# Optimization experiments

Measured on AMD Instinct MI355X. Metric: run time of the kernel, lower is better.

The kernel has to match this reference:

```python
import jax, jax.numpy as jnp
import numpy as np

N = 8192
D_IN = 512
D_OUT = 256
K = 16          # k_neighbor
ALPHA = 0.5
BETA = 1.0


def get_M(H, beta, k):
    """Cholesky-whitened kNN Gaussian-kernel graph, symmetrized. H: [N, d]."""
    d = H.shape[1]
    A = beta * jnp.eye(d, dtype=H.dtype) + H.T @ H            # [d, d]
    L = jnp.linalg.cholesky(A)                                # lower, A = L L^T
    # norm_covariance = H @ inv(L).T  ==  (L^{-1} H^T)^T
    Z = jax.scipy.linalg.solve_triangular(L, H.T, lower=True).T  # [N, d]
    sq = jnp.sum(Z * Z, axis=1)
    d2 = sq[:, None] + sq[None, :] - 2.0 * (Z @ Z.T)          # [N, N] squared dists
    neg_d2, idx = jax.lax.top_k(-d2, k)                       # k smallest
    vals = jnp.sqrt(jnp.clip(-neg_d2, 0.0))                   # [N, k]
    sigma = jnp.mean(vals)
    kern = jnp.exp(-(vals * vals) / (2.0 * sigma * sigma))
    n = Z.shape[0]
    rows = jnp.repeat(jnp.arange(n), k)
    M = jnp.zeros((n, n), Z.dtype).at[rows, idx.reshape(-1)].add(kern.reshape(-1))
    return 0.5 * (M + M.T)


def normalize_adj(M):
    deg = jnp.sum(M, axis=1)
    dis = jnp.where(deg > 0, deg ** -0.5, 0.0)
    return dis[:, None] * M * dis[None, :]


def setup_inputs() -> dict:
    key = jax.random.key(0)
    k1, k2, k3, k4 = jax.random.split(key, 4)
    lim1 = float(np.sqrt(6.0 / (D_IN + D_OUT)))
    lim2 = float(np.sqrt(6.0 / (D_OUT + D_OUT)))
    return {
        "x": jax.random.normal(k1, (N, D_IN), dtype=jnp.float32),
        "adj": jax.random.uniform(k2, (N, N), dtype=jnp.float32),
        "weight1": jax.random.uniform(k3, (D_IN, D_OUT), dtype=jnp.float32, minval=-lim1, maxval=lim1),
        "weight2": jax.random.uniform(k4, (D_OUT, D_OUT), dtype=jnp.float32, minval=-lim2, maxval=lim2),
    }


def reference(x, adj, weight1, weight2):
    # stage 1: build whitened kNN graph from detached x
    M1 = get_M(jax.lax.stop_gradient(x), BETA, K)
    new_adj = ALPHA * adj + normalize_adj(M1)
    out = jnp.tanh(new_adj @ (x @ weight1))                   # [N, D_OUT]
    # stage 2: rebuild graph from detached hidden, symmetrize weight2
    M2 = get_M(jax.lax.stop_gradient(out), BETA, K)
    new_adj2 = ALPHA * adj + normalize_adj(M2)
    w2_sym = 0.5 * (weight2 + weight2.T)
    out = jnp.tanh(new_adj2 @ (out @ w2_sym))
    return out
```

## Files before the change

### kernel.cpp

```cpp
#include <hip/hip_runtime.h>
#include <math.h>
#include <float.h>

#define N_TOT 8192
#define KNB 16
#define ALPHA 0.5f
#define PROWS 2048
#define NCH 8
#define KS 4

typedef short bf16x8 __attribute__((ext_vector_type(8)));
typedef float f32x4 __attribute__((ext_vector_type(4)));

__device__ inline unsigned short f2bf(float f) {
    unsigned u = __float_as_uint(f);
    u += 0x7fffu + ((u >> 16) & 1u);
    return (unsigned short)(u >> 16);
}
__device__ inline float bf2f(unsigned short h) {
    return __uint_as_float(((unsigned)h) << 16);
}

__global__ __launch_bounds__(256)
void k_ata2(const float* __restrict__ H, double* __restrict__ Apart, int d) {
    __shared__ float Ha[32][33], Hb[32][33];
    int tid = threadIdx.x, tx = tid&15, ty = tid>>4;
    int a0 = blockIdx.y*32, b0 = blockIdx.x*32;
    int n0b = blockIdx.z*(N_TOT/NCH);
    int lrow = tid>>3, lseg = tid&7;
    double acc[2][2];
    acc[0][0]=acc[0][1]=acc[1][0]=acc[1][1]=0.0;
    for (int n0 = n0b; n0 < n0b + N_TOT/NCH; n0 += 32) {
        float4 va = *(const float4*)&H[(long)(n0+lrow)*d + a0 + lseg*4];
        float4 vb = *(const float4*)&H[(long)(n0+lrow)*d + b0 + lseg*4];
        __syncthreads();
        Ha[lrow][lseg*4+0]=va.x; Ha[lrow][lseg*4+1]=va.y;
        Ha[lrow][lseg*4+2]=va.z; Ha[lrow][lseg*4+3]=va.w;
        Hb[lrow][lseg*4+0]=vb.x; Hb[lrow][lseg*4+1]=vb.y;
        Hb[lrow][lseg*4+2]=vb.z; Hb[lrow][lseg*4+3]=vb.w;
        __syncthreads();
        float f00=0.f,f01=0.f,f10=0.f,f11=0.f;
        #pragma unroll
        for (int nn = 0; nn < 32; ++nn) {
            float a0v = Ha[nn][ty*2], a1v = Ha[nn][ty*2+1];
            float b0v = Hb[nn][tx*2], b1v = Hb[nn][tx*2+1];
            f00 = fmaf(a0v,b0v,f00); f01 = fmaf(a0v,b1v,f01);
            f10 = fmaf(a1v,b0v,f10); f11 = fmaf(a1v,b1v,f11);
        }
        acc[0][0]+= (double)f00; acc[0][1]+= (double)f01;
        acc[1][0]+= (double)f10; acc[1][1]+= (double)f11;
    }
    long base = (long)blockIdx.z*d*d;
    #pragma unroll
    for (int i=0;i<2;++i)
        #pragma unroll
        for (int j=0;j<2;++j)
            Apart[base + (long)(a0+ty*2+i)*d + b0+tx*2+j] = acc[i][j];
}

__global__ __launch_bounds__(256)
void k_atared(const double* __restrict__ Apart, double* __restrict__ A,
              int d, double beta) {
    long idx = (long)blockIdx.x*256 + threadIdx.x;
    long dd = (long)d*d;
    double s = 0.0;
    for (int ch = 0; ch < NCH; ++ch) s += Apart[ch*dd + idx];
    int r = (int)(idx / d), c = (int)(idx % d);
    A[idx] = s + ((r==c) ? beta : 0.0);
}

__global__ __launch_bounds__(64)
void k_chol_diag(double* __restrict__ A, int d, int p0) {
    __shared__ double Ad[64][65];
    int r = threadIdx.x;
    for (int idx = r; idx < 64*64; idx += 64)
        Ad[idx>>6][idx&63] = A[(long)(p0+(idx>>6))*d + p0+(idx&63)];
    __syncthreads();
    for (int j = 0; j < 64; ++j) {
        double pj = sqrt(Ad[j][j]);
        double lrj = Ad[r][j] / pj;
        __syncthreads();
        if (r > j) Ad[r][j] = lrj;
        else if (r == j) Ad[j][j] = pj;
        __syncthreads();
        if (r > j)
            for (int k = j+1; k <= r; ++k)
                Ad[r][k] -= lrj * Ad[k][j];
        __syncthreads();
    }
    for (int idx = r; idx < 64*64; idx += 64) {
        int i = idx>>6, c = idx&63;
        A[(long)(p0+i)*d + p0+c] = (c <= i) ? Ad[i][c] : 0.0;
    }
}

__global__ __launch_bounds__(256)
void k_trsm(double* __restrict__ A, int d, int p0) {
    __shared__ double Lp[64][65];
    __shared__ double dg[64];
    int tid = threadIdx.x;
    for (int idx = tid; idx < 64*64; idx += 256) {
        int j = idx>>6, k = idx&63;
        double v = A[(long)(p0+j)*d + p0+k];
        Lp[j][k] = (j > k) ? v : 0.0;
        if (j == k) dg[j] = v;
    }
    __syncthreads();
    int r = p0 + 64 + blockIdx.x*256 + tid;
    if (r >= d) return;
    double* Ar = &A[(long)r*d + p0];
    double v[64];
    #pragma unroll
    for (int j = 0; j < 64; ++j) v[j] = Ar[j];
    #pragma unroll
    for (int k = 0; k < 64; ++k) {
        double lr = v[k] / dg[k];
        Ar[k] = lr;
        #pragma unroll
        for (int j = 0; j < 64; ++j) v[j] -= lr * Lp[j][k];
    }
}

__global__ __launch_bounds__(256)
void k_syrk(double* __restrict__ A, int d, int p0) {
    int t0 = p0 + 64;
    int r0 = t0 + blockIdx.y*64, c0 = t0 + blockIdx.x*64;
    __shared__ double Lr[64][33], Lc[64][33];
    int tid = threadIdx.x, tx = tid&15, ty = tid>>4;
    double acc[16];
    #pragma unroll
    for (int i=0;i<16;++i) acc[i]=0.0;
    for (int kc = 0; kc < 64; kc += 32) {
        for (int idx = tid; idx < 64*32; idx += 256) {
            int i = idx>>5, k = idx&31;
            Lr[i][k] = A[(long)(r0+i)*d + p0+kc+k];
            Lc[i][k] = A[(long)(c0+i)*d + p0+kc+k];
        }
        __syncthreads();
        for (int k = 0; k < 32; ++k) {
            double a[4], b[4];
            #pragma unroll
            for (int i=0;i<4;++i){ a[i]=Lr[ty*4+i][k]; b[i]=Lc[tx*4+i][k]; }
            #pragma unroll
            for (int i=0;i<4;++i)
                #pragma unroll
                for (int j=0;j<4;++j) acc[i*4+j] += a[i]*b[j];
        }
        __syncthreads();
    }
    #pragma unroll
    for (int i=0;i<4;++i)
        #pragma unroll
        for (int j=0;j<4;++j)
            A[(long)(r0+ty*4+i)*d + (c0+tx*4+j)] -= acc[i*4+j];
}

__global__ __launch_bounds__(64)
void k_dinv(const double* __restrict__ A, double* __restrict__ X, int d) {
    __shared__ double Lb[64][65];
    __shared__ double Yb[64][65];
    int b = blockIdx.x, c = threadIdx.x;
    for (int r = 0; r < 64; ++r) Lb[r][c] = A[(long)(b*64+r)*d + b*64+c];
    for (int r = 0; r < 64; ++r) Yb[r][c] = 0.0;
    __syncthreads();
    for (int i = 0; i < 64; ++i) {
        double s = (i==c) ? 1.0 : 0.0;
        for (int k = 0; k < i; ++k) s -= Lb[i][k]*Yb[k][c];
        Yb[i][c] = s / Lb[i][i];
    }
    __syncthreads();
    for (int r = 0; r < 64; ++r) X[(long)(b*64+r)*d + b*64+c] = Yb[r][c];
}

__global__ __launch_bounds__(256)
void k_xoff(const double* __restrict__ A, double* __restrict__ X, int d, int lev) {
    __shared__ double Lb[64][65];
    __shared__ double Xb[64][65];
    __shared__ double Sb[64][65];
    int j = blockIdx.x, i = j + lev;
    int tid = threadIdx.x, tx = tid&15, ty = tid>>4;
    double acc[4][4];
    #pragma unroll
    for (int m=0;m<4;++m)
        #pragma unroll
        for (int n=0;n<4;++n) acc[m][n]=0.0;
    for (int k = j; k < i; ++k) {
        __syncthreads();
        for (int idx = tid; idx < 64*64; idx += 256) {
            int r = idx>>6, cc = idx&63;
            Lb[r][cc] = A[(long)(i*64+r)*d + k*64+cc];
            Xb[r][cc] = X[(long)(k*64+r)*d + j*64+cc];
        }
        __syncthreads();
        for (int kk = 0; kk < 64; ++kk) {
            double a_[4], b_[4];
            #pragma unroll
            for (int m=0;m<4;++m) a_[m] = Lb[ty*4+m][kk];
            #pragma unroll
            for (int n=0;n<4;++n) b_[n] = Xb[kk][tx*4+n];
            #pragma unroll
            for (int m=0;m<4;++m)
                #pragma unroll
                for (int n=0;n<4;++n) acc[m][n] += a_[m]*b_[n];
        }
    }
    __syncthreads();
    #pragma unroll
    for (int m=0;m<4;++m)
        #pragma unroll
        for (int n=0;n<4;++n) Sb[ty*4+m][tx*4+n] = acc[m][n];
    for (int idx = tid; idx < 64*64; idx += 256) {
        int r = idx>>6, cc = idx&63;
        Lb[r][cc] = X[(long)(i*64+r)*d + i*64+cc];
    }
    __syncthreads();
    #pragma unroll
    for (int m=0;m<4;++m)
        #pragma unroll
        for (int n=0;n<4;++n) acc[m][n]=0.0;
    for (int kk = 0; kk < 64; ++kk) {
        double a_[4], b_[4];
        #pragma unroll
        for (int m=0;m<4;++m) a_[m] = Lb[ty*4+m][kk];
        #pragma unroll
        for (int n=0;n<4;++n) b_[n] = Sb[kk][tx*4+n];
        #pragma unroll
        for (int m=0;m<4;++m)
            #pragma unroll
            for (int n=0;n<4;++n) acc[m][n] += a_[m]*b_[n];
    }
    #pragma unroll
    for (int m=0;m<4;++m)
        #pragma unroll
        for (int n=0;n<4;++n)
            X[(long)(i*64+ty*4+m)*d + j*64+tx*4+n] = -acc[m][n];
}

__global__ __launch_bounds__(256)
void k_wtr(const double* __restrict__ X, double* __restrict__ W, int d, int shift) {
    int idx = blockIdx.x*256 + threadIdx.x;
    int k = idx >> shift, c = idx & (d-1);
    W[idx] = (k <= c) ? X[(long)c*d + k] : 0.0;
}

__global__ __launch_bounds__(256)
void k_hw(const float* __restrict__ H, const double* __restrict__ W,
          float* __restrict__ Z, int d) {
    __shared__ __align__(16) float Ht[32][68];
    __shared__ double Wt[32][66];
    int tid = threadIdx.x, tx = tid&15, ty = tid>>4;
    int r0 = blockIdx.y*64, c0 = blockIdx.x*64;
    double acc[4][4];
    #pragma unroll
    for (int i=0;i<4;++i)
        #pragma unroll
        for (int j=0;j<4;++j) acc[i][j]=0.0;
    for (int k0 = 0; k0 < d; k0 += 32) {
        {
            int row = tid>>2, koff = (tid&3)*8;
            const float* src = &H[(long)(r0+row)*d + k0+koff];
            float4 v0 = *(const float4*)src, v1 = *(const float4*)(src+4);
            Ht[koff+0][row]=v0.x; Ht[koff+1][row]=v0.y; Ht[koff+2][row]=v0.z; Ht[koff+3][row]=v0.w;
            Ht[koff+4][row]=v1.x; Ht[koff+5][row]=v1.y; Ht[koff+6][row]=v1.z; Ht[koff+7][row]=v1.w;
        }
        {
            int k = tid>>3, coff = (tid&7)*8;
            const double* src = &W[(long)(k0+k)*d + c0+coff];
            #pragma unroll
            for (int q=0;q<8;++q) Wt[k][coff+q] = src[q];
        }
        __syncthreads();
        #pragma unroll
        for (int k = 0; k < 32; ++k) {
            float4 av = *(const float4*)&Ht[k][ty*4];
            double a0=av.x, a1=av.y, a2=av.z, a3=av.w;
            double b[4];
            #pragma unroll
            for (int j=0;j<4;++j) b[j] = Wt[k][tx*4+j];
            #pragma unroll
            for (int j=0;j<4;++j) {
                acc[0][j] += a0*b[j]; acc[1][j] += a1*b[j];
                acc[2][j] += a2*b[j]; acc[3][j] += a3*b[j];
            }
        }
        __syncthreads();
    }
    #pragma unroll
    for (int i=0;i<4;++i)
        #pragma unroll
        for (int j=0;j<4;++j)
            Z[(long)(r0+ty*4+i)*d + c0+tx*4+j] = (float)acc[i][j];
}

__global__ __launch_bounds__(256)
void k_sq(const float* __restrict__ Z, float* __restrict__ sq, int d) {
    int row = blockIdx.x*4 + (threadIdx.x>>6);
    int lane = threadIdx.x&63;
    const float* z = &Z[(long)row*d];
    double s = 0.0;
    for (int c = lane; c < d; c += 64) { float v = z[c]; s += (double)v*v; }
    #pragma unroll
    for (int off=32; off>0; off>>=1) s += __shfl_down(s, off);
    if (lane==0) sq[row] = (float)s;
}

__global__ __launch_bounds__(256)
void k_bf16(const float* __restrict__ Z, unsigned short* __restrict__ Zh, long n) {
    long i = ((long)blockIdx.x*256 + threadIdx.x)*8;
    if (i >= n) return;
    float4 v0 = *(const float4*)&Z[i], v1 = *(const float4*)&Z[i+4];
    float z[8] = {v0.x,v0.y,v0.z,v0.w,v1.x,v1.y,v1.z,v1.w};
    __align__(16) unsigned short h[8];
    #pragma unroll
    for (int j=0;j<8;++j) h[j] = f2bf(z[j]);
    *(uint4*)&Zh[i] = *(const uint4*)h;
}

__global__ __launch_bounds__(256)
void k_gram(const unsigned short* __restrict__ Zh, const float* __restrict__ sq,
            float* __restrict__ d2, int d, int prow0) {
    __shared__ unsigned short At[128*64], Bt[128*64];
    int tid = threadIdx.x, w = tid>>6, lane = tid&63;
    int lr = lane&15, kg = lane>>4;
    int wr = w>>1, wc = w&1;
    int r0 = prow0 + blockIdx.y*128;
    int c0 = blockIdx.x*128;
    f32x4 acc[4][4];
    #pragma unroll
    for (int m=0;m<4;++m)
        #pragma unroll
        for (int n=0;n<4;++n) acc[m][n] = (f32x4){0.f,0.f,0.f,0.f};

    for (int k0 = 0; k0 < d; k0 += 64) {
        __syncthreads();
        #pragma unroll
        for (int ii=0; ii<4; ++ii) {
            int rbase = w*32 + ii*8;
            int grow = rbase + (lane>>3);
            int gg = (lane&7) ^ (grow&7);
            __builtin_amdgcn_global_load_lds((const void*)&Zh[(long)(r0+grow)*d + k0 + gg*8],
                                             (void*)&At[rbase*64], 16, 0, 0);
            __builtin_amdgcn_global_load_lds((const void*)&Zh[(long)(c0+grow)*d + k0 + gg*8],
                                             (void*)&Bt[rbase*64], 16, 0, 0);
        }
        __syncthreads();
        #pragma unroll
        for (int ks=0; ks<2; ++ks) {
            int gsw = ((ks<<2)|kg) ^ (lr&7);
            bf16x8 a_[4];
            #pragma unroll
            for (int m=0;m<4;++m) a_[m] = *(const bf16x8*)&At[(wr*64+m*16+lr)*64 + gsw*8];
            #pragma unroll
            for (int n=0;n<4;++n) {
                bf16x8 b_ = *(const bf16x8*)&Bt[(wc*64+n*16+lr)*64 + gsw*8];
                #pragma unroll
                for (int m=0;m<4;++m)
                    acc[m][n] = __builtin_amdgcn_mfma_f32_16x16x32_bf16(a_[m], b_, acc[m][n], 0,0,0);
            }
        }
    }
    float sr[4][4];
    #pragma unroll
    for (int m=0;m<4;++m)
        #pragma unroll
        for (int q=0;q<4;++q) sr[m][q] = sq[r0 + wr*64 + m*16 + kg*4 + q];
    #pragma unroll
    for (int n=0;n<4;++n) {
        int col = c0 + wc*64 + n*16 + lr;
        float sc = sq[col];
        #pragma unroll
        for (int m=0;m<4;++m) {
            int rloc = (r0 - prow0) + wr*64 + m*16 + kg*4;
            #pragma unroll
            for (int q=0;q<4;++q)
                d2[(long)(rloc+q)*N_TOT + col] = sr[m][q] + sc - 2.f*acc[m][n][q];
        }
    }
}

__global__ __launch_bounds__(256)
void k_sel(const float* __restrict__ d2, int* __restrict__ tI32, int prow0) {
    __shared__ float cbv[320];
    __shared__ int   cbi[320];
    __shared__ int   red[4];
    __shared__ int   cnt_s;
    __shared__ float fD[32];
    __shared__ int   fI[32];
    int tid = threadIdx.x, w = tid>>6, lane = tid&63;
    int row = blockIdx.x;
    const float* rp = &d2[(long)row*N_TOT];
    float v[32];
    #pragma unroll
    for (int j=0;j<8;++j) {
        float4 q = *(const float4*)&rp[j*1024 + tid*4];
        v[j*4+0]=q.x; v[j*4+1]=q.y; v[j*4+2]=q.z; v[j*4+3]=q.w;
    }
    unsigned u[32];
    #pragma unroll
    for (int i=0;i<32;++i) {
        unsigned b = __float_as_uint(v[i]);
        u[i] = (b & 0x80000000u) ? ~b : (b | 0x80000000u);
    }
    unsigned p = 0;
    for (int b = 31; b >= 0; --b) {
        unsigned t = p | (1u<<b);
        int c = 0;
        #pragma unroll
        for (int i=0;i<32;++i) c += (u[i] < t) ? 1 : 0;
        #pragma unroll
        for (int off=1; off<64; off<<=1) c += __shfl_xor(c, off);
        if (lane == 0) red[w] = c;
        __syncthreads();
        c = red[0]+red[1]+red[2]+red[3];
        if (c < 32) p = t;
        __syncthreads();
    }
    if (tid == 0) cnt_s = 0;
    __syncthreads();
    #pragma unroll
    for (int i=0;i<32;++i) {
        if (u[i] <= p) {
            int pos = atomicAdd(&cnt_s, 1);
            if (pos < 320) { cbv[pos] = v[i]; cbi[pos] = (i>>2)*1024 + tid*4 + (i&3); }
        }
    }
    __syncthreads();
    if (tid == 0) {
        int m = cnt_s; if (m > 320) m = 320;
        #pragma unroll
        for (int k=0;k<32;++k){ fD[k]=FLT_MAX; fI[k]=k; }
        for (int t = 0; t < m; ++t) {
            float dv = cbv[t]; int ci = cbi[t];
            float wd = fD[31]; int wi = fI[31];
            if (dv < wd || (dv == wd && ci < wi)) {
                int pos = 31;
                while (pos > 0) {
                    float pd_=fD[pos-1]; int pi_=fI[pos-1];
                    if (dv < pd_ || (dv == pd_ && ci < pi_)) { fD[pos]=pd_; fI[pos]=pi_; --pos; }
                    else break;
                }
                fD[pos]=dv; fI[pos]=ci;
            }
        }
        long rg = (long)(prow0 + row);
        #pragma unroll
        for (int k=0;k<32;++k) tI32[rg*32 + k] = fI[k];
    }
}

template<int D>
__global__ __launch_bounds__(256)
void k_refine(const float* __restrict__ Z, const float* __restrict__ sq,
              const int* __restrict__ tI32,
              float* __restrict__ tD, int* __restrict__ tI, double* sig_accum) {
    __shared__ float rD[4][32];
    __shared__ int   rI[4][32];
    __shared__ float bD[4][17];
    __shared__ int   bI[4][17];
    int wv = threadIdx.x>>6, lane = threadIdx.x&63;
    long row = (long)blockIdx.x*4 + wv;
    float zi[D/64];
    #pragma unroll
    for (int t=0;t<D/64;++t) zi[t] = Z[row*D + t*64 + lane];
    float sqi = sq[row];
    for (int c = 0; c < 32; ++c) {
        int j = tI32[row*32 + c];
        float dot = 0.f;
        #pragma unroll
        for (int t=0;t<D/64;++t) dot = fmaf(zi[t], Z[(long)j*D + t*64 + lane], dot);
        #pragma unroll
        for (int off=32; off>0; off>>=1) dot += __shfl_xor(dot, off);
        if (lane == 0) { rD[wv][c] = sqi + sq[j] - 2.f*dot; rI[wv][c] = j; }
    }
    if (lane == 0) {
        #pragma unroll
        for (int k=0;k<16;++k){ bD[wv][k]=FLT_MAX; bI[wv][k]=0x7fffffff; }
        for (int c = 0; c < 32; ++c) {
            float dv = rD[wv][c]; int ci = rI[wv][c];
            float wd = bD[wv][15]; int wi = bI[wv][15];
            if (dv < wd || (dv == wd && ci < wi)) {
                int pos = 15;
                while (pos > 0) {
                    float pd_ = bD[wv][pos-1]; int pi_ = bI[wv][pos-1];
                    if (dv < pd_ || (dv == pd_ && ci < pi_)) {
                        bD[wv][pos]=pd_; bI[wv][pos]=pi_; --pos;
                    } else break;
                }
                bD[wv][pos]=dv; bI[wv][pos]=ci;
            }
        }
        double ps = 0.0;
        #pragma unroll
        for (int k=0;k<16;++k) {
            float dv = bD[wv][k];
            tD[row*16+k] = dv; tI[row*16+k] = bI[wv][k];
            ps += sqrt((double)fmaxf(dv, 0.f));
        }
        atomicAdd(sig_accum, ps);
    }
}

__global__ void k_sigfin(const double* __restrict__ sig_accum, float* __restrict__ inv2s2) {
    double s = sig_accum[0] / (double)(N_TOT*KNB);
    inv2s2[0] = (float)(1.0/(2.0*s*s));
}

__global__ __launch_bounds__(256)
void k_kern(const float* __restrict__ tD, const int* __restrict__ tI,
            const float* __restrict__ inv2s2,
            float* __restrict__ kern, float* __restrict__ deg) {
    int e = blockIdx.x*256 + threadIdx.x;
    int i = e>>4;
    float d2 = fmaxf(tD[e], 0.f);
    float kv = expf(-d2 * inv2s2[0]);
    kern[e] = kv;
    atomicAdd(&deg[i], 0.5f*kv);
    atomicAdd(&deg[tI[e]], 0.5f*kv);
}

__global__ __launch_bounds__(256)
void k_dis(const float* __restrict__ deg, float* __restrict__ dis) {
    int i = blockIdx.x*256 + threadIdx.x;
    float v = deg[i];
    dis[i] = (v > 0.f) ? (1.0f/sqrtf(v)) : 0.f;
}

__global__ __launch_bounds__(256)
void k_wedge(const float* __restrict__ kern, const int* __restrict__ tI,
             const float* __restrict__ dis, float* __restrict__ wout) {
    int e = blockIdx.x*256 + threadIdx.x;
    wout[e] = 0.5f * kern[e] * dis[tI[e]];
}

__global__ __launch_bounds__(256)
void k_count(const int* __restrict__ tI, int* __restrict__ cnt) {
    int e = blockIdx.x*256 + threadIdx.x;
    atomicAdd(&cnt[tI[e]], 1);
}

__global__ __launch_bounds__(1024)
void k_scan(const int* __restrict__ cnt, int* __restrict__ rowstart) {
    __shared__ int buf[1024];
    __shared__ int carry;
    int tid = threadIdx.x;
    if (tid==0) carry = 0;
    __syncthreads();
    for (int base = 0; base < N_TOT; base += 1024) {
        int v = cnt[base+tid];
        buf[tid]=v; __syncthreads();
        for (int off=1; off<1024; off<<=1) {
            int t = (tid>=off)? buf[tid-off] : 0; __syncthreads();
            buf[tid]+=t; __syncthreads();
        }
        rowstart[base+tid] = carry + buf[tid] - v;
        __syncthreads();
        if (tid==1023) carry += buf[1023];
        __syncthreads();
    }
    if (tid==0) rowstart[N_TOT] = carry;
}

__global__ __launch_bounds__(256)
void k_fill(const int* __restrict__ tI, const float* __restrict__ kern,
            const float* __restrict__ dis,
            const int* __restrict__ rowstart, int* __restrict__ c2,
            int* __restrict__ in_src, float* __restrict__ in_w) {
    int e = blockIdx.x*256 + threadIdx.x;
    int i = e>>4;
    int j = tI[e];
    int pos = atomicAdd(&c2[j], 1);
    int dst = rowstart[j] + pos;
    in_src[dst] = i; in_w[dst] = 0.5f*kern[e]*dis[i];
}

__global__ __launch_bounds__(256)
void k_gemm(const float* __restrict__ A, const float* __restrict__ B,
            float* __restrict__ C, int M, int N, int Kd, float scale) {
    __shared__ __align__(16) float At[16][68];
    __shared__ __align__(16) float Bt[16][68];
    int tid = threadIdx.x, tx = tid&15, ty = tid>>4;
    int r0 = blockIdx.y*64, c0 = blockIdx.x*64;
    float acc[4][4];
    #pragma unroll
    for (int i=0;i<4;++i)
        #pragma unroll
        for (int j=0;j<4;++j) acc[i][j]=0.f;
    for (int k0 = 0; k0 < Kd; k0 += 16) {
        {
            int row = tid>>2, koff = (tid&3)*4;
            float4 v = *(const float4*)&A[(long)(r0+row)*Kd + k0+koff];
            At[koff+0][row]=v.x; At[koff+1][row]=v.y; At[koff+2][row]=v.z; At[koff+3][row]=v.w;
        }
        {
            int k = tid>>4, coff = (tid&15)*4;
            float4 v = *(const float4*)&B[(long)(k0+k)*N + c0+coff];
            *(float4*)&Bt[k][coff] = v;
        }
        __syncthreads();
        #pragma unroll
        for (int k=0;k<16;++k) {
            float4 a = *(const float4*)&At[k][ty*4];
            float4 b = *(const float4*)&Bt[k][tx*4];
            float ar[4] = {a.x,a.y,a.z,a.w};
            float br[4] = {b.x,b.y,b.z,b.w};
            #pragma unroll
            for (int i=0;i<4;++i)
                #pragma unroll
                for (int j=0;j<4;++j) acc[i][j] = fmaf(ar[i], br[j], acc[i][j]);
        }
        __syncthreads();
    }
    #pragma unroll
    for (int i=0;i<4;++i)
        #pragma unroll
        for (int j=0;j<4;++j)
            C[(long)(r0+ty*4+i)*N + c0+tx*4+j] = scale*acc[i][j];
}

__global__ __launch_bounds__(256)
void k_prepPT(const float* __restrict__ P, unsigned short* __restrict__ PTsh,
              unsigned short* __restrict__ PTsl) {
    __shared__ float tile[64][65];
    int r0 = blockIdx.y*64;
    int c0 = blockIdx.x*64;
    int t = threadIdx.x;
    {
        int row = t>>2, cseg = t&3;
        #pragma unroll
        for (int i=0;i<4;++i) {
            float4 v = *(const float4*)&P[(long)(r0+row)*256 + c0 + cseg*16 + i*4];
            tile[row][cseg*16+i*4+0]=v.x; tile[row][cseg*16+i*4+1]=v.y;
            tile[row][cseg*16+i*4+2]=v.z; tile[row][cseg*16+i*4+3]=v.w;
        }
    }
    __syncthreads();
    {
        int col = t>>2, rseg = t&3;
        int c = c0 + col;
        __align__(16) unsigned short hs[16], ls[16];
        #pragma unroll
        for (int i=0;i<16;++i) {
            float z = tile[rseg*16+i][col];
            hs[i] = f2bf(z);
            ls[i] = f2bf(z - bf2f(hs[i]));
        }
        #pragma unroll
        for (int half=0; half<2; ++half) {
            int gl = rseg*2 + half;
            int gs = gl ^ (c&7);
            long dst = (long)c*N_TOT + r0 + gs*8;
            *(uint4*)&PTsh[dst] = *(const uint4*)&hs[half*8];
            *(uint4*)&PTsl[dst] = *(const uint4*)&ls[half*8];
        }
    }
}

__global__ __launch_bounds__(256)
void k_adjP3(const float* __restrict__ adj, const unsigned short* __restrict__ PTsh,
             const unsigned short* __restrict__ PTsl, float* __restrict__ part) {
    __shared__ unsigned short Ah[64*64], Al[64*64];
    __shared__ unsigned short Bh[128*64], Bl[128*64];
    int tid = threadIdx.x, w = tid>>6, lane = tid&63;
    int lr = lane&15, kg = lane>>4;
    int r0 = blockIdx.y*64;
    int c0 = blockIdx.x*128;
    int kbeg = blockIdx.z*(N_TOT/KS), kend = kbeg + N_TOT/KS;
    f32x4 acc[8];
    #pragma unroll
    for (int fc=0; fc<8; ++fc) acc[fc] = (f32x4){0.f,0.f,0.f,0.f};

    int arow = tid>>2, aseg = tid&3;
    float4 va[4];
    {
        const float* asrc = &adj[(long)(r0+arow)*N_TOT + kbeg + aseg*16];
        #pragma unroll
        for (int i=0;i<4;++i) va[i] = *(const float4*)&asrc[i*4];
    }
    for (int k0 = kbeg; k0 < kend; k0 += 64) {
        __syncthreads();
        #pragma unroll
        for (int i=0;i<4;++i) {
            float z[4] = {va[i].x, va[i].y, va[i].z, va[i].w};
            __align__(8) unsigned short h[4], l[4];
            #pragma unroll
            for (int j=0;j<4;++j) {
                h[j] = f2bf(z[j]);
                l[j] = f2bf(z[j] - bf2f(h[j]));
            }
            int col = aseg*16 + i*4;
            int g = col>>3, sub = col&7;
            int off = arow*128 + ((g ^ (arow&7))*16) + sub*2;
            *(ushort4*)((char*)Ah + off) = *(const ushort4*)h;
            *(ushort4*)((char*)Al + off) = *(const ushort4*)l;
        }
        #pragma unroll
        for (int ii=0; ii<4; ++ii) {
            int rbase = w*32 + ii*8;
            int grow = rbase + (lane>>3);
            long src = (long)(c0+grow)*N_TOT + k0 + (lane&7)*8;
            __builtin_amdgcn_global_load_lds((const void*)&PTsh[src], (void*)&Bh[rbase*64], 16, 0, 0);
            __builtin_amdgcn_global_load_lds((const void*)&PTsl[src], (void*)&Bl[rbase*64], 16, 0, 0);
        }
        __syncthreads();
        if (k0 + 64 < kend) {
            const float* asrc = &adj[(long)(r0+arow)*N_TOT + k0 + 64 + aseg*16];
            #pragma unroll
            for (int i=0;i<4;++i) va[i] = *(const float4*)&asrc[i*4];
        }
        #pragma unroll
        for (int ks=0; ks<2; ++ks) {
            int gsw = ((ks<<2)|kg) ^ (lr&7);
            bf16x8 ah = *(const bf16x8*)&Ah[(w*16+lr)*64 + gsw*8];
            bf16x8 al = *(const bf16x8*)&Al[(w*16+lr)*64 + gsw*8];
            #pragma unroll
            for (int fc=0; fc<8; ++fc) {
                bf16x8 bh = *(const bf16x8*)&Bh[(fc*16+lr)*64 + gsw*8];
                bf16x8 bl = *(const bf16x8*)&Bl[(fc*16+lr)*64 + gsw*8];
                acc[fc] = __builtin_amdgcn_mfma_f32_16x16x32_bf16(ah, bh, acc[fc], 0,0,0);
                acc[fc] = __builtin_amdgcn_mfma_f32_16x16x32_bf16(ah, bl, acc[fc], 0,0,0);
                acc[fc] = __builtin_amdgcn_mfma_f32_16x16x32_bf16(al, bh, acc[fc], 0,0,0);
            }
        }
    }
    long base = (long)blockIdx.z*N_TOT*256;
    #pragma unroll
    for (int fc=0; fc<8; ++fc)
        #pragma unroll
        for (int q=0; q<4; ++q) {
            int rg = r0 + w*16 + kg*4 + q;
            int cg = c0 + fc*16 + lr;
            part[base + (long)rg*256 + cg] = acc[fc][q];
        }
}

__global__ __launch_bounds__(256)
void k_adjred(const float* __restrict__ part, float* __restrict__ preS, float scale) {
    long i4 = ((long)blockIdx.x*256 + threadIdx.x)*4;
    long n = (long)N_TOT*256;
    float4 a = *(const float4*)&part[i4];
    float4 b = *(const float4*)&part[n + i4];
    float4 c = *(const float4*)&part[2*n + i4];
    float4 d = *(const float4*)&part[3*n + i4];
    float4 o;
    o.x = scale*(((a.x + b.x) + c.x) + d.x);
    o.y = scale*(((a.y + b.y) + c.y) + d.y);
    o.z = scale*(((a.z + b.z) + c.z) + d.z);
    o.w = scale*(((a.w + b.w) + c.w) + d.w);
    *(float4*)&preS[i4] = o;
}

__global__ __launch_bounds__(256)
void k_wsym(const float* __restrict__ w2, float* __restrict__ w2s) {
    int i = blockIdx.x, j = threadIdx.x;
    w2s[i*256+j] = 0.5f*(w2[i*256+j] + w2[j*256+i]);
}

__global__ __launch_bounds__(256)
void k_spmm_tanh(const float* __restrict__ P, const float* __restrict__ preS,
                 const float* __restrict__ wout, const int* __restrict__ tI,
                 const float* __restrict__ dis, const int* __restrict__ rowstart,
                 const int* __restrict__ in_src, const float* __restrict__ in_w,
                 float* __restrict__ out) {
    int i = blockIdx.x, c = threadIdx.x;
    float a0=0.f, a1=0.f, a2=0.f, a3=0.f;
    #pragma unroll
    for (int k = 0; k < 16; k += 4) {
        int e = i*16+k;
        int j0 = tI[e+0], j1 = tI[e+1], j2 = tI[e+2], j3 = tI[e+3];
        float w0 = wout[e+0], w1 = wout[e+1], w2 = wout[e+2], w3 = wout[e+3];
        a0 = fmaf(w0, P[(long)j0*256 + c], a0);
        a1 = fmaf(w1, P[(long)j1*256 + c], a1);
        a2 = fmaf(w2, P[(long)j2*256 + c], a2);
        a3 = fmaf(w3, P[(long)j3*256 + c], a3);
    }
    int s0 = rowstart[i], s1 = rowstart[i+1];
    int t = s0;
    for (; t + 4 <= s1; t += 4) {
        int j0 = in_src[t+0], j1 = in_src[t+1], j2 = in_src[t+2], j3 = in_src[t+3];
        float w0 = in_w[t+0], w1 = in_w[t+1], w2 = in_w[t+2], w3 = in_w[t+3];
        a0 = fmaf(w0, P[(long)j0*256 + c], a0);
        a1 = fmaf(w1, P[(long)j1*256 + c], a1);
        a2 = fmaf(w2, P[(long)j2*256 + c], a2);
        a3 = fmaf(w3, P[(long)j3*256 + c], a3);
    }
    for (; t < s1; ++t)
        a0 = fmaf(in_w[t], P[(long)in_src[t]*256 + c], a0);
    float acc = (a0 + a1) + (a2 + a3);
    float pre = preS[(long)i*256+c] + dis[i]*acc;
    out[(long)i*256+c] = tanhf(pre);
}

extern "C" void kernel_launch(void* const* d_in, const int* in_sizes, int n_in,
                              void* d_out, int out_size, void* d_ws, size_t ws_size,
                              hipStream_t stream) {
    const float* x   = (const float*)d_in[0];
    const float* adj = (const float*)d_in[1];
    const float* w1  = (const float*)d_in[2];
    const float* w2  = (const float*)d_in[3];

    char* ws = (char*)d_ws;
    size_t off = 0;
    auto alloc = [&](size_t bytes){ size_t o = off; off += (bytes+255)&~(size_t)255; return o; };
    double* A      = (double*)(ws + alloc((size_t)512*512*8));
    double* W      = (double*)(ws + alloc((size_t)512*512*8));
    double* Xb     = (double*)(ws + alloc((size_t)512*512*8));
    double* Apart  = (double*)(ws + alloc((size_t)NCH*512*512*8));
    double* sigacc = (double*)(ws + alloc(256));
    float*  inv2s2 = (float*)(ws + alloc(256));
    float*  bigZ   = (float*)(ws + alloc((size_t)N_TOT*512*4));
    unsigned short* Zh   = (unsigned short*)(ws + alloc((size_t)N_TOT*512*2));
    unsigned short* PTsh = (unsigned short*)(ws + alloc((size_t)256*N_TOT*2));
    unsigned short* PTsl = (unsigned short*)(ws + alloc((size_t)256*N_TOT*2));
    float*  d2buf  = (float*)(ws + alloc((size_t)PROWS*N_TOT*4));
    float*  part   = (float*)(ws + alloc((size_t)KS*N_TOT*256*4));
    float*  sq     = (float*)(ws + alloc((size_t)N_TOT*4));
    int*    tI32   = (int*)  (ws + alloc((size_t)N_TOT*32*4));
    float*  tD     = (float*)(ws + alloc((size_t)N_TOT*16*4));
    int*    tI     = (int*)  (ws + alloc((size_t)N_TOT*16*4));
    float*  kern   = (float*)(ws + alloc((size_t)N_TOT*16*4));
    float*  wout   = (float*)(ws + alloc((size_t)N_TOT*16*4));
    float*  deg    = (float*)(ws + alloc((size_t)N_TOT*4));
    float*  dis    = (float*)(ws + alloc((size_t)N_TOT*4));
    int*    cnt    = (int*)  (ws + alloc((size_t)N_TOT*4));
    int*    rowstart=(int*)  (ws + alloc((size_t)(N_TOT+1)*4));
    int*    c2     = (int*)  (ws + alloc((size_t)N_TOT*4));
    int*    in_src = (int*)  (ws + alloc((size_t)N_TOT*16*4));
    float*  in_w   = (float*)(ws + alloc((size_t)N_TOT*16*4));
    float*  out1   = (float*)(ws + alloc((size_t)N_TOT*256*4));
    float*  w2s    = (float*)(ws + alloc((size_t)256*256*4));
    float*  P      = bigZ;
    float*  preS   = bigZ + (size_t)N_TOT*256;

    auto run_stage = [&](const float* H, int d, const float* Bmat, float* outBuf) {
        int nb = d/64;
        int shift = (d == 512) ? 9 : 8;
        k_ata2<<<dim3(d/32, d/32, NCH), 256, 0, stream>>>(H, Apart, d);
        k_atared<<<d*d/256, 256, 0, stream>>>(Apart, A, d, 1.0);
        for (int p0 = 0; p0 < d; p0 += 64) {
            k_chol_diag<<<1, 64, 0, stream>>>(A, d, p0);
            int rem = d - p0 - 64;
            if (rem > 0) {
                k_trsm<<<(rem+255)/256, 256, 0, stream>>>(A, d, p0);
                k_syrk<<<dim3(rem/64, rem/64), 256, 0, stream>>>(A, d, p0);
            }
        }
        k_dinv<<<nb, 64, 0, stream>>>(A, Xb, d);
        for (int lev = 1; lev < nb; ++lev)
            k_xoff<<<nb - lev, 256, 0, stream>>>(A, Xb, d, lev);
        k_wtr<<<d*d/256, 256, 0, stream>>>(Xb, W, d, shift);
        k_hw<<<dim3(d/64, N_TOT/64), 256, 0, stream>>>(H, W, bigZ, d);
        k_sq<<<N_TOT/4, 256, 0, stream>>>(bigZ, sq, d);
        k_bf16<<<(int)(((long)N_TOT*d)/(256*8)), 256, 0, stream>>>(bigZ, Zh, (long)N_TOT*d);
        for (int pr = 0; pr < N_TOT; pr += PROWS) {
            k_gram<<<dim3(N_TOT/128, PROWS/128), 256, 0, stream>>>(Zh, sq, d2buf, d, pr);
            k_sel<<<PROWS, 256, 0, stream>>>(d2buf, tI32, pr);
        }
        hipMemsetAsync(sigacc, 0, 8, stream);
        if (d == 512)
            k_refine<512><<<N_TOT/4, 256, 0, stream>>>(bigZ, sq, tI32, tD, tI, sigacc);
        else
            k_refine<256><<<N_TOT/4, 256, 0, stream>>>(bigZ, sq, tI32, tD, tI, sigacc);
        k_sigfin<<<1, 1, 0, stream>>>(sigacc, inv2s2);
        hipMemsetAsync(deg, 0, N_TOT*4, stream);
        k_kern<<<N_TOT*16/256, 256, 0, stream>>>(tD, tI, inv2s2, kern, deg);
        k_dis<<<N_TOT/256, 256, 0, stream>>>(deg, dis);
        k_wedge<<<N_TOT*16/256, 256, 0, stream>>>(kern, tI, dis, wout);
        hipMemsetAsync(cnt, 0, N_TOT*4, stream);
        k_count<<<N_TOT*16/256, 256, 0, stream>>>(tI, cnt);
        k_scan<<<1, 1024, 0, stream>>>(cnt, rowstart);
        hipMemsetAsync(c2, 0, N_TOT*4, stream);
        k_fill<<<N_TOT*16/256, 256, 0, stream>>>(tI, kern, dis, rowstart, c2, in_src, in_w);
        k_gemm<<<dim3(256/64, N_TOT/64), 256, 0, stream>>>(H, Bmat, P, N_TOT, 256, d, 1.0f);
        k_prepPT<<<dim3(4, N_TOT/64), 256, 0, stream>>>(P, PTsh, PTsl);
        k_adjP3<<<dim3(2, N_TOT/64, KS), 256, 0, stream>>>(adj, PTsh, PTsl, part);
        k_adjred<<<(N_TOT*256)/(256*4), 256, 0, stream>>>(part, preS, ALPHA);
        k_spmm_tanh<<<N_TOT, 256, 0, stream>>>(P, preS, wout, tI, dis, rowstart,
                                               in_src, in_w, outBuf);
    };

    run_stage(x, 512, w1, out1);
    k_wsym<<<256, 256, 0, stream>>>(w2, w2s);
    run_stage(out1, 256, w2s, (float*)d_out);
}
```

Before: 5.386 ms.

## Move H·W projection to split-bf16 MFMA, widen adj split-K, pair refine dots

Replaces the FP32 SIMT GEMM that computes P = H·W with an MFMA kernel that emulates FP32 precision. Both operands are split into bf16 high and low parts and three bf16 products are accumulated. It adds a split kernel and reuses a generalized transpose/split kernel to prepare the operands. It also doubles the split-K factor of the adj·P kernel (with a generic reduction loop), and processes two candidate neighbors per iteration in the refine kernel for more memory-level parallelism. The trade-offs are extra conversion passes and workspace for the split operands, plus more partial-sum traffic from the larger split-K.

```diff
diff --git a/kernel.cpp b/kernel.cpp
--- a/kernel.cpp
+++ b/kernel.cpp
@@ -7,7 +7,7 @@
 #define ALPHA 0.5f
 #define PROWS 2048
 #define NCH 8
-#define KS 4
+#define KS 8
 
 typedef short bf16x8 __attribute__((ext_vector_type(8)));
 typedef float f32x4 __attribute__((ext_vector_type(4)));
@@ -314,6 +314,23 @@
     #pragma unroll
     for (int j=0;j<8;++j) h[j] = f2bf(z[j]);
     *(uint4*)&Zh[i] = *(const uint4*)h;
+}
+
+__global__ __launch_bounds__(256)
+void k_split(const float* __restrict__ in, unsigned short* __restrict__ ho,
+             unsigned short* __restrict__ lo, long n) {
+    long i = ((long)blockIdx.x*256 + threadIdx.x)*8;
+    if (i >= n) return;
+    float4 v0 = *(const float4*)&in[i], v1 = *(const float4*)&in[i+4];
+    float z[8] = {v0.x,v0.y,v0.z,v0.w,v1.x,v1.y,v1.z,v1.w};
+    __align__(16) unsigned short h[8], l[8];
+    #pragma unroll
+    for (int j=0;j<8;++j) {
+        h[j] = f2bf(z[j]);
+        l[j] = f2bf(z[j] - bf2f(h[j]));
+    }
+    *(uint4*)&ho[i] = *(const uint4*)h;
+    *(uint4*)&lo[i] = *(const uint4*)l;
 }
 
 __global__ __launch_bounds__(256)
@@ -463,14 +480,23 @@
     #pragma unroll
     for (int t=0;t<D/64;++t) zi[t] = Z[row*D + t*64 + lane];
     float sqi = sq[row];
-    for (int c = 0; c < 32; ++c) {
-        int j = tI32[row*32 + c];
-        float dot = 0.f;
-        #pragma unroll
-        for (int t=0;t<D/64;++t) dot = fmaf(zi[t], Z[(long)j*D + t*64 + lane], dot);
-        #pragma unroll
-        for (int off=32; off>0; off>>=1) dot += __shfl_xor(dot, off);
-        if (lane == 0) { rD[wv][c] = sqi + sq[j] - 2.f*dot; rI[wv][c] = j; }
+    for (int c = 0; c < 32; c += 2) {
+        int j0 = tI32[row*32 + c], j1 = tI32[row*32 + c + 1];
+        float dot0 = 0.f, dot1 = 0.f;
+        #pragma unroll
+        for (int t=0;t<D/64;++t) {
+            dot0 = fmaf(zi[t], Z[(long)j0*D + t*64 + lane], dot0);
+            dot1 = fmaf(zi[t], Z[(long)j1*D + t*64 + lane], dot1);
+        }
+        #pragma unroll
+        for (int off=32; off>0; off>>=1) {
+            dot0 += __shfl_xor(dot0, off);
+            dot1 += __shfl_xor(dot1, off);
+        }
+        if (lane == 0) {
+            rD[wv][c]   = sqi + sq[j0] - 2.f*dot0; rI[wv][c]   = j0;
+            rD[wv][c+1] = sqi + sq[j1] - 2.f*dot1; rI[wv][c+1] = j1;
+        }
     }
     if (lane == 0) {
         #pragma unroll
@@ -574,52 +600,8 @@
 }
 
 __global__ __launch_bounds__(256)
-void k_gemm(const float* __restrict__ A, const float* __restrict__ B,
-            float* __restrict__ C, int M, int N, int Kd, float scale) {
-    __shared__ __align__(16) float At[16][68];
-    __shared__ __align__(16) float Bt[16][68];
-    int tid = threadIdx.x, tx = tid&15, ty = tid>>4;
-    int r0 = blockIdx.y*64, c0 = blockIdx.x*64;
-    float acc[4][4];
-    #pragma unroll
-    for (int i=0;i<4;++i)
-        #pragma unroll
-        for (int j=0;j<4;++j) acc[i][j]=0.f;
-    for (int k0 = 0; k0 < Kd; k0 += 16) {
-        {
-            int row = tid>>2, koff = (tid&3)*4;
-            float4 v = *(const float4*)&A[(long)(r0+row)*Kd + k0+koff];
-            At[koff+0][row]=v.x; At[koff+1][row]=v.y; At[koff+2][row]=v.z; At[koff+3][row]=v.w;
-        }
-        {
-            int k = tid>>4, coff = (tid&15)*4;
-            float4 v = *(const float4*)&B[(long)(k0+k)*N + c0+coff];
-            *(float4*)&Bt[k][coff] = v;
-        }
-        __syncthreads();
-        #pragma unroll
-        for (int k=0;k<16;++k) {
-            float4 a = *(const float4*)&At[k][ty*4];
-            float4 b = *(const float4*)&Bt[k][tx*4];
-            float ar[4] = {a.x,a.y,a.z,a.w};
-            float br[4] = {b.x,b.y,b.z,b.w};
-            #pragma unroll
-            for (int i=0;i<4;++i)
-                #pragma unroll
-                for (int j=0;j<4;++j) acc[i][j] = fmaf(ar[i], br[j], acc[i][j]);
-        }
-        __syncthreads();
-    }
-    #pragma unroll
-    for (int i=0;i<4;++i)
-        #pragma unroll
-        for (int j=0;j<4;++j)
-            C[(long)(r0+ty*4+i)*N + c0+tx*4+j] = scale*acc[i][j];
-}
-
-__global__ __launch_bounds__(256)
-void k_prepPT(const float* __restrict__ P, unsigned short* __restrict__ PTsh,
-              unsigned short* __restrict__ PTsl) {
+void k_prepT(const float* __restrict__ S, unsigned short* __restrict__ Th,
+             unsigned short* __restrict__ Tl, int outStride) {
     __shared__ float tile[64][65];
     int r0 = blockIdx.y*64;
     int c0 = blockIdx.x*64;
@@ -628,7 +610,7 @@
         int row = t>>2, cseg = t&3;
         #pragma unroll
         for (int i=0;i<4;++i) {
-            float4 v = *(const float4*)&P[(long)(r0+row)*256 + c0 + cseg*16 + i*4];
+            float4 v = *(const float4*)&S[(long)(r0+row)*256 + c0 + cseg*16 + i*4];
             tile[row][cseg*16+i*4+0]=v.x; tile[row][cseg*16+i*4+1]=v.y;
             tile[row][cseg*16+i*4+2]=v.z; tile[row][cseg*16+i*4+3]=v.w;
         }
@@ -648,9 +630,75 @@
         for (int half=0; half<2; ++half) {
             int gl = rseg*2 + half;
             int gs = gl ^ (c&7);
-            long dst = (long)c*N_TOT + r0 + gs*8;
-            *(uint4*)&PTsh[dst] = *(const uint4*)&hs[half*8];
-            *(uint4*)&PTsl[dst] = *(const uint4*)&ls[half*8];
+            long dst = (long)c*outStride + r0 + gs*8;
+            *(uint4*)&Th[dst] = *(const uint4*)&hs[half*8];
+            *(uint4*)&Tl[dst] = *(const uint4*)&ls[half*8];
+        }
+    }
+}
+
+__global__ __launch_bounds__(256)
+void k_hb(const unsigned short* __restrict__ Hh, const unsigned short* __restrict__ Hl,
+          const unsigned short* __restrict__ BTh, const unsigned short* __restrict__ BTl,
+          float* __restrict__ C, int d) {
+    __shared__ unsigned short Ah[128*64], Al[128*64], Bh[128*64], Bl[128*64];
+    int tid = threadIdx.x, w = tid>>6, lane = tid&63;
+    int lr = lane&15, kg = lane>>4;
+    int wr = w>>1, wc = w&1;
+    int r0 = blockIdx.y*128;
+    int c0 = blockIdx.x*128;
+    f32x4 acc[4][4];
+    #pragma unroll
+    for (int m=0;m<4;++m)
+        #pragma unroll
+        for (int n=0;n<4;++n) acc[m][n] = (f32x4){0.f,0.f,0.f,0.f};
+
+    for (int k0 = 0; k0 < d; k0 += 64) {
+        __syncthreads();
+        #pragma unroll
+        for (int ii=0; ii<4; ++ii) {
+            int rbase = w*32 + ii*8;
+            int grow = rbase + (lane>>3);
+            int gg = (lane&7) ^ (grow&7);
+            long asrc = (long)(r0+grow)*d + k0 + gg*8;
+            __builtin_amdgcn_global_load_lds((const void*)&Hh[asrc], (void*)&Ah[rbase*64], 16, 0, 0);
+            __builtin_amdgcn_global_load_lds((const void*)&Hl[asrc], (void*)&Al[rbase*64], 16, 0, 0);
+            long bsrc = (long)(c0+grow)*d + k0 + (lane&7)*8;
+            __builtin_amdgcn_global_load_lds((const void*)&BTh[bsrc], (void*)&Bh[rbase*64], 16, 0, 0);
+            __builtin_amdgcn_global_load_lds((const void*)&BTl[bsrc], (void*)&Bl[rbase*64], 16, 0, 0);
+        }
+        __syncthreads();
+        #pragma unroll
+        for (int ks=0; ks<2; ++ks) {
+            int gsw = ((ks<<2)|kg) ^ (lr&7);
+            bf16x8 ah[4], al[4];
+            #pragma unroll
+            for (int m=0;m<4;++m) {
+                ah[m] = *(const bf16x8*)&Ah[(wr*64+m*16+lr)*64 + gsw*8];
+                al[m] = *(const bf16x8*)&Al[(wr*64+m*16+lr)*64 + gsw*8];
+            }
+            #pragma unroll
+            for (int n=0;n<4;++n) {
+                bf16x8 bh = *(const bf16x8*)&Bh[(wc*64+n*16+lr)*64 + gsw*8];
+                bf16x8 bl = *(const bf16x8*)&Bl[(wc*64+n*16+lr)*64 + gsw*8];
+                #pragma unroll
+                for (int m=0;m<4;++m) {
+                    acc[m][n] = __builtin_amdgcn_mfma_f32_16x16x32_bf16(ah[m], bh, acc[m][n], 0,0,0);
+                    acc[m][n] = __builtin_amdgcn_mfma_f32_16x16x32_bf16(ah[m], bl, acc[m][n], 0,0,0);
+                    acc[m][n] = __builtin_amdgcn_mfma_f32_16x16x32_bf16(al[m], bh, acc[m][n], 0,0,0);
+                }
+            }
+        }
+    }
+    #pragma unroll
+    for (int n=0;n<4;++n) {
+        int col = c0 + wc*64 + n*16 + lr;
+        #pragma unroll
+        for (int m=0;m<4;++m) {
+            int rg = r0 + wr*64 + m*16 + kg*4;
+            #pragma unroll
+            for (int q=0;q<4;++q)
+                C[(long)(rg+q)*256 + col] = acc[m][n][q];
         }
     }
 }
@@ -737,15 +785,12 @@
 void k_adjred(const float* __restrict__ part, float* __restrict__ preS, float scale) {
     long i4 = ((long)blockIdx.x*256 + threadIdx.x)*4;
     long n = (long)N_TOT*256;
-    float4 a = *(const float4*)&part[i4];
-    float4 b = *(const float4*)&part[n + i4];
-    float4 c = *(const float4*)&part[2*n + i4];
-    float4 d = *(const float4*)&part[3*n + i4];
-    float4 o;
-    o.x = scale*(((a.x + b.x) + c.x) + d.x);
-    o.y = scale*(((a.y + b.y) + c.y) + d.y);
-    o.z = scale*(((a.z + b.z) + c.z) + d.z);
-    o.w = scale*(((a.w + b.w) + c.w) + d.w);
+    float sx=0.f, sy=0.f, sz=0.f, sw=0.f;
+    for (int ch = 0; ch < KS; ++ch) {
+        float4 a = *(const float4*)&part[(long)ch*n + i4];
+        sx += a.x; sy += a.y; sz += a.z; sw += a.w;
+    }
+    float4 o; o.x = scale*sx; o.y = scale*sy; o.z = scale*sz; o.w = scale*sw;
     *(float4*)&preS[i4] = o;
 }
 
@@ -809,6 +854,10 @@
     float*  inv2s2 = (float*)(ws + alloc(256));
     float*  bigZ   = (float*)(ws + alloc((size_t)N_TOT*512*4));
     unsigned short* Zh   = (unsigned short*)(ws + alloc((size_t)N_TOT*512*2));
+    unsigned short* Hh   = (unsigned short*)(ws + alloc((size_t)N_TOT*512*2));
+    unsigned short* Hl   = (unsigned short*)(ws + alloc((size_t)N_TOT*512*2));
+    unsigned short* BTh  = (unsigned short*)(ws + alloc((size_t)256*512*2));
+    unsigned short* BTl  = (unsigned short*)(ws + alloc((size_t)256*512*2));
     unsigned short* PTsh = (unsigned short*)(ws + alloc((size_t)256*N_TOT*2));
     unsigned short* PTsl = (unsigned short*)(ws + alloc((size_t)256*N_TOT*2));
     float*  d2buf  = (float*)(ws + alloc((size_t)PROWS*N_TOT*4));
@@ -870,8 +919,10 @@
         k_scan<<<1, 1024, 0, stream>>>(cnt, rowstart);
         hipMemsetAsync(c2, 0, N_TOT*4, stream);
         k_fill<<<N_TOT*16/256, 256, 0, stream>>>(tI, kern, dis, rowstart, c2, in_src, in_w);
-        k_gemm<<<dim3(256/64, N_TOT/64), 256, 0, stream>>>(H, Bmat, P, N_TOT, 256, d, 1.0f);
-        k_prepPT<<<dim3(4, N_TOT/64), 256, 0, stream>>>(P, PTsh, PTsl);
+        k_split<<<(int)(((long)N_TOT*d)/(256*8)), 256, 0, stream>>>(H, Hh, Hl, (long)N_TOT*d);
+        k_prepT<<<dim3(4, d/64), 256, 0, stream>>>(Bmat, BTh, BTl, d);
+        k_hb<<<dim3(2, N_TOT/128), 256, 0, stream>>>(Hh, Hl, BTh, BTl, P, d);
+        k_prepT<<<dim3(4, N_TOT/64), 256, 0, stream>>>(P, PTsh, PTsl, N_TOT);
         k_adjP3<<<dim3(2, N_TOT/64, KS), 256, 0, stream>>>(adj, PTsh, PTsl, part);
         k_adjred<<<(N_TOT*256)/(256*4), 256, 0, stream>>>(part, preS, ALPHA);
         k_spmm_tanh<<<N_TOT, 256, 0, stream>>>(P, preS, wout, tI, dis, rowstart,
```

Result: no change. 5.376 ms (-0.2%).
